# Optimization experiments

Hardware: AMD Instinct MI355X
Metric: run time of the kernel (lower is better)

## Reference

```python
import jax, jax.numpy as jnp
import numpy as np

ALPHA = 32.0
LN_EPS = 1e-5

def _cdist(a, b):
    # a: [C, M, K], b: [C, N, K] -> [C, M, N] euclidean distances
    d2 = (jnp.sum(a * a, -1)[:, :, None]
          + jnp.sum(b * b, -1)[:, None, :]
          - 2.0 * jnp.einsum('cmk,cnk->cmn', a, b))
    return jnp.sqrt(jnp.maximum(d2, 1e-12))

def setup_inputs() -> dict:
    key = jax.random.key(0)
    k1, k2 = jax.random.split(key)
    B, D, H, W, C = 8, 16, 28, 28, 256
    CN, SS = 128, 28 * 28
    x = jax.random.normal(k1, (B, D, H, W, C), dtype=jnp.float32)
    ln_weight = jnp.ones((C,), dtype=jnp.float32)
    ln_bias = jnp.zeros((C,), dtype=jnp.float32)
    cluster_center = jax.random.uniform(k2, (C, CN, SS), dtype=jnp.float32)
    return {"x": x, "ln_weight": ln_weight, "ln_bias": ln_bias,
            "cluster_center": cluster_center}

def reference(x, ln_weight, ln_bias, cluster_center):
    B, D, H, W, C = x.shape
    CN = cluster_center.shape[1]
    # LayerNorm over last dim (feature_dim)
    mu = jnp.mean(x, -1, keepdims=True)
    var = jnp.mean(jnp.square(x - mu), -1, keepdims=True)
    xn = (x - mu) * jax.lax.rsqrt(var + LN_EPS) * ln_weight + ln_bias
    # B D H W C -> C (B D) (H W)
    x_re = jnp.transpose(xn, (4, 0, 1, 2, 3)).reshape(C, B * D, H * W)
    soft_assign = _cdist(x_re, cluster_center)          # [C, B*D, CN]
    # C (B D) CN -> B D C CN
    x_distance = jnp.transpose(soft_assign.reshape(C, B, D, CN), (1, 2, 0, 3))
    # NegSoftAssign: exp(-alpha*(x - min)) normalized == softmax(-alpha*x)
    x_distance_assign = jax.nn.softmax(-ALPHA * x_distance, axis=-1)
    cluster_dist = _cdist(cluster_center, cluster_center)  # [C, CN, CN]
    return (x_distance, x_distance_assign, cluster_dist)
```

## Files before the change

kernel.cpp:

```cpp
#include <hip/hip_runtime.h>
#include <hip/hip_bf16.h>
#include <math.h>

#define C_DIM 256
#define BD    128
#define HW    784
#define CN    128
#define KPAD  832
#define KTILES 26
#define CC_BLOCKS 2048

typedef short bf16x8 __attribute__((ext_vector_type(8)));
typedef float f32x4 __attribute__((ext_vector_type(4)));

__device__ inline ushort f2b(float f) {
  unsigned u = __float_as_uint(f);
  unsigned r = (u + 0x7FFFu + ((u >> 16) & 1u)) >> 16;
  return (ushort)r;
}

__global__ __launch_bounds__(256, 5) void prep_kernel(
    const float* __restrict__ x, const float* __restrict__ lnw,
    const float* __restrict__ lnb, const float* __restrict__ cc,
    ushort* __restrict__ xre, ushort* __restrict__ ccb) {
  __shared__ __align__(16) ushort btile[256 * 32];
  const int t = threadIdx.x, bid = blockIdx.x;
  const int w = t >> 6, lane = t & 63;
  const int q = lane >> 4, l = lane & 15;

  if (bid < CC_BLOCKS) {
    const int c = bid >> 3;
    const int r = (bid & 7) * 16 + w * 4 + q;
    const float4* src = (const float4*)(cc + ((size_t)c * CN + r) * HW);
    ushort* dst = ccb + ((size_t)c * CN + r) * KPAD;
    float4 v[13];
#pragma unroll
    for (int i = 0; i < 13; ++i) {
      if (i < 12 || l < 4) v[i] = src[i * 16 + l];
    }
#pragma unroll
    for (int i = 0; i < 13; ++i) {
      if (i < 12 || l < 4) {
        ushort4 o;
        o.x = f2b(v[i].x); o.y = f2b(v[i].y);
        o.z = f2b(v[i].z); o.w = f2b(v[i].w);
        *(ushort4*)(dst + (i * 16 + l) * 4) = o;
      }
    }
    if (l < 12) *(ushort4*)(dst + 784 + l * 4) = make_ushort4(0, 0, 0, 0);
    return;
  }

  const int idx = bid - CC_BLOCKS;
  const int bx = idx % 26;
  const int bd = idx / 26;
  const int hw0 = bx * 32;

  if (bx == 25) {
#pragma unroll
    for (int i = 0; i < 8; ++i) {
      int c = w * 64 + i * 8 + (lane >> 3);
      int ho = (lane & 7) * 4;
      *(uint2*)(xre + (size_t)c * (BD * KPAD) + (size_t)bd * KPAD + hw0 + ho) =
          make_uint2(0u, 0u);
    }
    return;
  }

  const bool half = (bx == 24);
  const int ngroups = half ? 1 : 2;
  const int rpw = ngroups * 4;
  const int msk = (l & 7) << 2;

  if (half) {
    int rp2 = (16 + w * 4 + q) ^ msk;
#pragma unroll
    for (int s = 0; s < 4; ++s)
#pragma unroll
      for (int j = 0; j < 4; ++j)
        btile[(s * 64 + l * 4 + j) * 32 + rp2] = 0;
  }

  float4 wv[4], bv[4];
#pragma unroll
  for (int s = 0; s < 4; ++s) {
    wv[s] = *(const float4*)(lnw + s * 64 + l * 4);
    bv[s] = *(const float4*)(lnb + s * 64 + l * 4);
  }
  const float* xb = x + ((size_t)bd * HW + hw0) * 256 + l * 4;

#define LOADG(V, g)                                                            \
  do {                                                                         \
    int r_ = w * rpw + (g) * 4 + q;                                            \
    _Pragma("unroll") for (int s = 0; s < 4; ++s)                              \
        V[s] = *(const float4*)(xb + (size_t)r_ * 256 + s * 64);               \
  } while (0)

#define PROC(V, g)                                                             \
  do {                                                                         \
    int r_ = w * rpw + (g) * 4 + q;                                            \
    float sum = 0.f, sq = 0.f;                                                 \
    _Pragma("unroll") for (int s = 0; s < 4; ++s) {                            \
      sum += V[s].x + V[s].y + V[s].z + V[s].w;                                \
      sq = fmaf(V[s].x, V[s].x, sq); sq = fmaf(V[s].y, V[s].y, sq);            \
      sq = fmaf(V[s].z, V[s].z, sq); sq = fmaf(V[s].w, V[s].w, sq);            \
    }                                                                          \
    for (int off = 1; off <= 8; off <<= 1) {                                   \
      sum += __shfl_xor(sum, off, 64);                                         \
      sq  += __shfl_xor(sq, off, 64);                                          \
    }                                                                          \
    float mu = sum * (1.f / 256.f);                                            \
    float var = fmaf(-mu, mu, sq * (1.f / 256.f));                             \
    float sc = rsqrtf(var + 1e-5f);                                            \
    int rp_ = r_ ^ msk;                                                        \
    _Pragma("unroll") for (int s = 0; s < 4; ++s) {                            \
      float y0 = (V[s].x - mu) * sc * wv[s].x + bv[s].x;                       \
      float y1 = (V[s].y - mu) * sc * wv[s].y + bv[s].y;                       \
      float y2 = (V[s].z - mu) * sc * wv[s].z + bv[s].z;                       \
      float y3 = (V[s].w - mu) * sc * wv[s].w + bv[s].w;                       \
      int c_ = s * 64 + l * 4;                                                 \
      btile[(c_ + 0) * 32 + rp_] = f2b(y0);                                    \
      btile[(c_ + 1) * 32 + rp_] = f2b(y1);                                    \
      btile[(c_ + 2) * 32 + rp_] = f2b(y2);                                    \
      btile[(c_ + 3) * 32 + rp_] = f2b(y3);                                    \
    }                                                                          \
  } while (0)

  float4 va[4], vb[4];
  LOADG(va, 0);
  if (ngroups > 1) {
    LOADG(vb, 1);
    PROC(va, 0);
    PROC(vb, 1);
  } else {
    PROC(va, 0);
  }
#undef LOADG
#undef PROC
  __syncthreads();
#pragma unroll
  for (int i = 0; i < 8; ++i) {
    int c = w * 64 + i * 8 + (lane >> 3);
    int xw = ((c >> 2) & 7) << 2;
    int ho = (lane & 7) * 4;
    uint2 val = *(const uint2*)&btile[c * 32 + (ho ^ xw)];
    *(uint2*)(xre + (size_t)c * (BD * KPAD) + (size_t)bd * KPAD + hw0 + ho) = val;
  }
}

__global__ __launch_bounds__(256, 2) void gemm_fused_kernel(
    const ushort* __restrict__ xre, const ushort* __restrict__ ccb,
    float* __restrict__ out_d, float* __restrict__ out_s,
    float* __restrict__ out_c) {
  __shared__ __align__(16) ushort At[2][2048];
  __shared__ __align__(16) ushort Bt[2][4096];
  __shared__ float an_l[64], bn_l[128];
  const int bid = blockIdx.x;
  const int xcd = bid & 7, i6 = bid >> 3;
  const int c = xcd * 32 + (i6 >> 1);
  const int h = i6 & 1;
  const int t = threadIdx.x, w = t >> 6, lane = t & 63;
  const int quad = lane >> 4, ln = lane & 15;
  const ushort* Ag = xre + (size_t)c * (128 * KPAD) + (size_t)(h * 64) * KPAD;
  const ushort* Bg = ccb + (size_t)c * (128 * KPAD);

  f32x4 accx[8], accc[8];
  f32x4 accd  = f32x4{0.f, 0.f, 0.f, 0.f};
  f32x4 accbd = f32x4{0.f, 0.f, 0.f, 0.f};
#pragma unroll
  for (int j = 0; j < 8; ++j) {
    accx[j] = f32x4{0.f, 0.f, 0.f, 0.f};
    accc[j] = f32x4{0.f, 0.f, 0.f, 0.f};
  }

  const int srow = t >> 2, scq = (t & 3) ^ (srow & 3);
  const ushort* gA  = Ag + (size_t)srow * KPAD + scq * 8;
  const ushort* gB1 = Bg + (size_t)srow * KPAD + scq * 8;
  const ushort* gB2 = Bg + (size_t)(srow + 64) * KPAD + scq * 8;

  const int m = w * 16 + ln;
  const int aoff  = (m * 4 + (quad ^ (m & 3))) * 8;
  const int aroff = ((h * 64 + m) * 4 + (quad ^ (m & 3))) * 8;
  const int nD = (1 - h) * 64 + w * 16 + ln;
  const int bdoff = (nD * 4 + (quad ^ (nD & 3))) * 8;
  int boff[8];
#pragma unroll
  for (int j = 0; j < 8; ++j) {
    int n = j * 16 + ln;
    boff[j] = (n * 4 + (quad ^ (n & 3))) * 8;
  }

#define ISSUE(k, p)                                                            \
  do {                                                                         \
    int kb = (k) * 32;                                                         \
    __builtin_amdgcn_global_load_lds(                                          \
        (const __attribute__((address_space(1))) unsigned int*)(gA + kb),      \
        (__attribute__((address_space(3))) unsigned int*)&At[p][t * 8], 16, 0, 0); \
    __builtin_amdgcn_global_load_lds(                                          \
        (const __attribute__((address_space(1))) unsigned int*)(gB1 + kb),     \
        (__attribute__((address_space(3))) unsigned int*)&Bt[p][t * 8], 16, 0, 0); \
    __builtin_amdgcn_global_load_lds(                                          \
        (const __attribute__((address_space(1))) unsigned int*)(gB2 + kb),     \
        (__attribute__((address_space(3))) unsigned int*)&Bt[p][t * 8 + 2048], 16, 0, 0); \
  } while (0)

  ISSUE(0, 0);
  for (int k0 = 0; k0 < KTILES; ++k0) {
    __syncthreads();
    if (k0 < KTILES - 1) ISSUE(k0 + 1, (k0 + 1) & 1);
    const int p = k0 & 1;
    bf16x8 af  = *(const bf16x8*)&At[p][aoff];
    bf16x8 ar  = *(const bf16x8*)&Bt[p][aroff];
    bf16x8 bdr = *(const bf16x8*)&Bt[p][bdoff];
    accd  = __builtin_amdgcn_mfma_f32_16x16x32_bf16(af, af, accd, 0, 0, 0);
    accbd = __builtin_amdgcn_mfma_f32_16x16x32_bf16(bdr, bdr, accbd, 0, 0, 0);
#pragma unroll
    for (int j = 0; j < 8; ++j) {
      bf16x8 bfj = *(const bf16x8*)&Bt[p][boff[j]];
      accx[j] = __builtin_amdgcn_mfma_f32_16x16x32_bf16(af, bfj, accx[j], 0, 0, 0);
      accc[j] = __builtin_amdgcn_mfma_f32_16x16x32_bf16(ar, bfj, accc[j], 0, 0, 0);
    }
  }
#undef ISSUE

  if ((ln >> 2) == quad) {
#pragma unroll
    for (int r2 = 0; r2 < 4; ++r2)
      if (r2 == (ln & 3)) {
        an_l[w * 16 + ln] = accd[r2];
        bn_l[(1 - h) * 64 + w * 16 + ln] = accbd[r2];
      }
#pragma unroll
    for (int j = 0; j < 8; ++j)
      if (j == h * 4 + w) {
#pragma unroll
        for (int r2 = 0; r2 < 4; ++r2)
          if (r2 == (ln & 3))
            bn_l[h * 64 + w * 16 + ln] = accc[j][r2];
      }
  }
  __syncthreads();

  float cn[8];
#pragma unroll
  for (int j = 0; j < 8; ++j) cn[j] = bn_l[j * 16 + ln];
  float rx[4], rc[4];
#pragma unroll
  for (int r = 0; r < 4; ++r) {
    rx[r] = an_l[w * 16 + quad * 4 + r];
    rc[r] = bn_l[h * 64 + w * 16 + quad * 4 + r];
  }
#pragma unroll
  for (int r = 0; r < 4; ++r) {
    int mr = h * 64 + w * 16 + quad * 4 + r;
    float* ob = out_c + (size_t)c * (128 * 128) + (size_t)mr * 128;
#pragma unroll
    for (int j = 0; j < 8; ++j) {
      float d2 = rc[r] + cn[j] - 2.f * accc[j][r];
      ob[j * 16 + ln] = sqrtf(fmaxf(d2, 1e-12f));
    }
  }
#pragma unroll
  for (int r = 0; r < 4; ++r) {
    int mr = h * 64 + w * 16 + quad * 4 + r;
    float dr[8];
#pragma unroll
    for (int j = 0; j < 8; ++j) {
      float d2 = rx[r] + cn[j] - 2.f * accx[j][r];
      dr[j] = sqrtf(fmaxf(d2, 1e-12f));
    }
    float* ob = out_d + ((size_t)mr * 256 + c) * 128;
#pragma unroll
    for (int j = 0; j < 8; ++j) ob[j * 16 + ln] = dr[j];
    float mn = dr[0];
#pragma unroll
    for (int j = 1; j < 8; ++j) mn = fminf(mn, dr[j]);
    for (int off = 1; off <= 8; off <<= 1) mn = fminf(mn, __shfl_xor(mn, off, 64));
    float e[8], s = 0.f;
#pragma unroll
    for (int j = 0; j < 8; ++j) { e[j] = __expf(-32.f * (dr[j] - mn)); s += e[j]; }
    for (int off = 1; off <= 8; off <<= 1) s += __shfl_xor(s, off, 64);
    float inv = 1.f / s;
    float* os = out_s + ((size_t)mr * 256 + c) * 128;
#pragma unroll
    for (int j = 0; j < 8; ++j) os[j * 16 + ln] = e[j] * inv;
  }
}

extern "C" void kernel_launch(void* const* d_in, const int* in_sizes, int n_in,
                              void* d_out, int out_size, void* d_ws, size_t ws_size,
                              hipStream_t stream) {
  const float* x   = (const float*)d_in[0];
  const float* lnw = (const float*)d_in[1];
  const float* lnb = (const float*)d_in[2];
  const float* cc  = (const float*)d_in[3];
  float* out   = (float*)d_out;
  float* out_d = out;
  float* out_s = out + 4194304;
  float* out_c = out + 8388608;

  ushort* xre_b = (ushort*)d_ws;
  ushort* cc_b  = xre_b + 27262976;

  prep_kernel<<<5376, 256, 0, stream>>>(x, lnw, lnb, cc, xre_b, cc_b);
  gemm_fused_kernel<<<512, 256, 0, stream>>>(xre_b, cc_b, out_d, out_s, out_c);
}
```

Before: 306.0 us.

## Triple-buffer GEMM loads with explicit waitcnt and widen prep tiles to 64 columns

Result: faster. 297.3 us (-2.8%).

```diff
diff --git a/kernel.cpp b/kernel.cpp
--- a/kernel.cpp
+++ b/kernel.cpp
@@ -8,7 +8,6 @@
 #define CN    128
 #define KPAD  832
 #define KTILES 26
-#define CC_BLOCKS 2048
 
 typedef short bf16x8 __attribute__((ext_vector_type(8)));
 typedef float f32x4 __attribute__((ext_vector_type(4)));
@@ -19,16 +18,16 @@
   return (ushort)r;
 }
 
-__global__ __launch_bounds__(256, 5) void prep_kernel(
+__global__ __launch_bounds__(256, 4) void prep_kernel(
     const float* __restrict__ x, const float* __restrict__ lnw,
     const float* __restrict__ lnb, const float* __restrict__ cc,
     ushort* __restrict__ xre, ushort* __restrict__ ccb) {
-  __shared__ __align__(16) ushort btile[256 * 32];
+  __shared__ __align__(16) ushort btile[256 * 64];
   const int t = threadIdx.x, bid = blockIdx.x;
   const int w = t >> 6, lane = t & 63;
   const int q = lane >> 4, l = lane & 15;
 
-  if (bid < CC_BLOCKS) {
+  if (bid < 2048) {
     const int c = bid >> 3;
     const int r = (bid & 7) * 16 + w * 4 + q;
     const float4* src = (const float4*)(cc + ((size_t)c * CN + r) * HW);
@@ -51,36 +50,19 @@
     return;
   }
 
-  const int idx = bid - CC_BLOCKS;
-  const int bx = idx % 26;
-  const int bd = idx / 26;
-  const int hw0 = bx * 32;
-
-  if (bx == 25) {
-#pragma unroll
-    for (int i = 0; i < 8; ++i) {
-      int c = w * 64 + i * 8 + (lane >> 3);
-      int ho = (lane & 7) * 4;
-      *(uint2*)(xre + (size_t)c * (BD * KPAD) + (size_t)bd * KPAD + hw0 + ho) =
-          make_uint2(0u, 0u);
-    }
-    return;
-  }
-
-  const bool half = (bx == 24);
-  const int ngroups = half ? 1 : 2;
+  const int idx = bid - 2048;
+  const int bx = idx % 13;
+  const int bd = idx / 13;
+  const int hw0 = bx * 64;
+  const bool last = (bx == 12);
+  const int ngroups = last ? 1 : 4;
   const int rpw = ngroups * 4;
-  const int msk = (l & 7) << 2;
-
-  if (half) {
-    int rp2 = (16 + w * 4 + q) ^ msk;
-#pragma unroll
-    for (int s = 0; s < 4; ++s)
-#pragma unroll
-      for (int j = 0; j < 4; ++j)
-        btile[(s * 64 + l * 4 + j) * 32 + rp2] = 0;
-  }
-
+  const int xr2 = (l & 12) | ((l & 3) << 4);
+  if (last) {
+    int xf = ((t >> 2) & 12) ^ ((t & 12) << 2);
+    for (int r = 16; r < 64; r += 4)
+      *(ushort4*)&btile[t * 64 + (r ^ xf)] = make_ushort4(0, 0, 0, 0);
+  }
   float4 wv[4], bv[4];
 #pragma unroll
   for (int s = 0; s < 4; ++s) {
@@ -112,17 +94,17 @@
     float mu = sum * (1.f / 256.f);                                            \
     float var = fmaf(-mu, mu, sq * (1.f / 256.f));                             \
     float sc = rsqrtf(var + 1e-5f);                                            \
-    int rp_ = r_ ^ msk;                                                        \
+    int rp_ = r_ ^ xr2;                                                        \
     _Pragma("unroll") for (int s = 0; s < 4; ++s) {                            \
       float y0 = (V[s].x - mu) * sc * wv[s].x + bv[s].x;                       \
       float y1 = (V[s].y - mu) * sc * wv[s].y + bv[s].y;                       \
       float y2 = (V[s].z - mu) * sc * wv[s].z + bv[s].z;                       \
       float y3 = (V[s].w - mu) * sc * wv[s].w + bv[s].w;                       \
       int c_ = s * 64 + l * 4;                                                 \
-      btile[(c_ + 0) * 32 + rp_] = f2b(y0);                                    \
-      btile[(c_ + 1) * 32 + rp_] = f2b(y1);                                    \
-      btile[(c_ + 2) * 32 + rp_] = f2b(y2);                                    \
-      btile[(c_ + 3) * 32 + rp_] = f2b(y3);                                    \
+      btile[(c_ + 0) * 64 + rp_] = f2b(y0);                                    \
+      btile[(c_ + 1) * 64 + rp_] = f2b(y1);                                    \
+      btile[(c_ + 2) * 64 + rp_] = f2b(y2);                                    \
+      btile[(c_ + 3) * 64 + rp_] = f2b(y3);                                    \
     }                                                                          \
   } while (0)
 
@@ -131,7 +113,11 @@
   if (ngroups > 1) {
     LOADG(vb, 1);
     PROC(va, 0);
+    LOADG(va, 2);
     PROC(vb, 1);
+    LOADG(vb, 3);
+    PROC(va, 2);
+    PROC(vb, 3);
   } else {
     PROC(va, 0);
   }
@@ -139,11 +125,11 @@
 #undef PROC
   __syncthreads();
 #pragma unroll
-  for (int i = 0; i < 8; ++i) {
-    int c = w * 64 + i * 8 + (lane >> 3);
-    int xw = ((c >> 2) & 7) << 2;
-    int ho = (lane & 7) * 4;
-    uint2 val = *(const uint2*)&btile[c * 32 + (ho ^ xw)];
+  for (int i = 0; i < 16; ++i) {
+    int c = w * 64 + i * 4 + (lane >> 4);
+    int xw = ((c >> 2) & 12) ^ ((c & 12) << 2);
+    int ho = (lane & 15) * 4;
+    uint2 val = *(const uint2*)&btile[c * 64 + (ho ^ xw)];
     *(uint2*)(xre + (size_t)c * (BD * KPAD) + (size_t)bd * KPAD + hw0 + ho) = val;
   }
 }
@@ -152,8 +138,8 @@
     const ushort* __restrict__ xre, const ushort* __restrict__ ccb,
     float* __restrict__ out_d, float* __restrict__ out_s,
     float* __restrict__ out_c) {
-  __shared__ __align__(16) ushort At[2][2048];
-  __shared__ __align__(16) ushort Bt[2][4096];
+  __shared__ __align__(16) ushort At[3][2048];
+  __shared__ __align__(16) ushort Bt[3][4096];
   __shared__ float an_l[64], bn_l[128];
   const int bid = blockIdx.x;
   const int xcd = bid & 7, i6 = bid >> 3;
@@ -205,13 +191,23 @@
   } while (0)
 
   ISSUE(0, 0);
+  ISSUE(1, 1);
   for (int k0 = 0; k0 < KTILES; ++k0) {
-    __syncthreads();
-    if (k0 < KTILES - 1) ISSUE(k0 + 1, (k0 + 1) & 1);
-    const int p = k0 & 1;
+    const int p = k0 % 3;
+    if (k0 < KTILES - 2) {
+      ISSUE(k0 + 2, (k0 + 2) % 3);
+      asm volatile("s_waitcnt vmcnt(6)" ::: "memory");
+    } else if (k0 == KTILES - 2) {
+      asm volatile("s_waitcnt vmcnt(3)" ::: "memory");
+    } else {
+      asm volatile("s_waitcnt vmcnt(0)" ::: "memory");
+    }
+    __builtin_amdgcn_s_barrier();
+    __builtin_amdgcn_sched_barrier(0);
     bf16x8 af  = *(const bf16x8*)&At[p][aoff];
     bf16x8 ar  = *(const bf16x8*)&Bt[p][aroff];
     bf16x8 bdr = *(const bf16x8*)&Bt[p][bdoff];
+    __builtin_amdgcn_s_setprio(1);
     accd  = __builtin_amdgcn_mfma_f32_16x16x32_bf16(af, af, accd, 0, 0, 0);
     accbd = __builtin_amdgcn_mfma_f32_16x16x32_bf16(bdr, bdr, accbd, 0, 0, 0);
 #pragma unroll
@@ -220,9 +216,13 @@
       accx[j] = __builtin_amdgcn_mfma_f32_16x16x32_bf16(af, bfj, accx[j], 0, 0, 0);
       accc[j] = __builtin_amdgcn_mfma_f32_16x16x32_bf16(ar, bfj, accc[j], 0, 0, 0);
     }
+    __builtin_amdgcn_s_setprio(0);
+    asm volatile("s_waitcnt lgkmcnt(0)" ::: "memory");
+    __builtin_amdgcn_s_barrier();
   }
 #undef ISSUE
 
+  __syncthreads();
   if ((ln >> 2) == quad) {
 #pragma unroll
     for (int r2 = 0; r2 < 4; ++r2)
@@ -302,6 +302,6 @@
   ushort* xre_b = (ushort*)d_ws;
   ushort* cc_b  = xre_b + 27262976;
 
-  prep_kernel<<<5376, 256, 0, stream>>>(x, lnw, lnb, cc, xre_b, cc_b);
+  prep_kernel<<<3712, 256, 0, stream>>>(x, lnw, lnb, cc, xre_b, cc_b);
   gemm_fused_kernel<<<512, 256, 0, stream>>>(xre_b, cc_b, out_d, out_s, out_c);
 }
```

## Split LayerNorm into stats pass and wide-tile apply/transpose kernel

Applied to the files above, without the earlier changes.

New measurement: 318.3 us. +4.0%, slower.

```diff
diff --git a/kernel.cpp b/kernel.cpp
--- a/kernel.cpp
+++ b/kernel.cpp
@@ -8,7 +8,6 @@
 #define CN    128
 #define KPAD  832
 #define KTILES 26
-#define CC_BLOCKS 2048
 
 typedef short bf16x8 __attribute__((ext_vector_type(8)));
 typedef float f32x4 __attribute__((ext_vector_type(4)));
@@ -19,16 +18,14 @@
   return (ushort)r;
 }
 
-__global__ __launch_bounds__(256, 5) void prep_kernel(
-    const float* __restrict__ x, const float* __restrict__ lnw,
-    const float* __restrict__ lnb, const float* __restrict__ cc,
-    ushort* __restrict__ xre, ushort* __restrict__ ccb) {
-  __shared__ __align__(16) ushort btile[256 * 32];
+__global__ __launch_bounds__(256) void stats_cc_kernel(
+    const float* __restrict__ x, const float* __restrict__ cc,
+    float2* __restrict__ stats, ushort* __restrict__ ccb) {
   const int t = threadIdx.x, bid = blockIdx.x;
   const int w = t >> 6, lane = t & 63;
   const int q = lane >> 4, l = lane & 15;
 
-  if (bid < CC_BLOCKS) {
+  if (bid < 2048) {
     const int c = bid >> 3;
     const int r = (bid & 7) * 16 + w * 4 + q;
     const float4* src = (const float4*)(cc + ((size_t)c * CN + r) * HW);
@@ -51,54 +48,21 @@
     return;
   }
 
-  const int idx = bid - CC_BLOCKS;
-  const int bx = idx % 26;
-  const int bd = idx / 26;
-  const int hw0 = bx * 32;
-
-  if (bx == 25) {
-#pragma unroll
-    for (int i = 0; i < 8; ++i) {
-      int c = w * 64 + i * 8 + (lane >> 3);
-      int ho = (lane & 7) * 4;
-      *(uint2*)(xre + (size_t)c * (BD * KPAD) + (size_t)bd * KPAD + hw0 + ho) =
-          make_uint2(0u, 0u);
-    }
-    return;
-  }
-
-  const bool half = (bx == 24);
-  const int ngroups = half ? 1 : 2;
-  const int rpw = ngroups * 4;
-  const int msk = (l & 7) << 2;
-
-  if (half) {
-    int rp2 = (16 + w * 4 + q) ^ msk;
-#pragma unroll
-    for (int s = 0; s < 4; ++s)
-#pragma unroll
-      for (int j = 0; j < 4; ++j)
-        btile[(s * 64 + l * 4 + j) * 32 + rp2] = 0;
-  }
-
-  float4 wv[4], bv[4];
-#pragma unroll
-  for (int s = 0; s < 4; ++s) {
-    wv[s] = *(const float4*)(lnw + s * 64 + l * 4);
-    bv[s] = *(const float4*)(lnb + s * 64 + l * 4);
-  }
-  const float* xb = x + ((size_t)bd * HW + hw0) * 256 + l * 4;
-
-#define LOADG(V, g)                                                            \
+  const int sb = bid - 2048;
+  const int bd = sb / 7, tile = sb % 7;
+  const int hwbase = tile * 112;
+
+#define LOADP(V, p)                                                            \
   do {                                                                         \
-    int r_ = w * rpw + (g) * 4 + q;                                            \
-    _Pragma("unroll") for (int s = 0; s < 4; ++s)                              \
-        V[s] = *(const float4*)(xb + (size_t)r_ * 256 + s * 64);               \
+    int hw_ = hwbase + (p) * 16 + w * 4 + q;                                   \
+    const float* rp = x + ((size_t)bd * HW + hw_) * 256 + l * 4;               \
+    V[0] = *(const float4*)rp;       V[1] = *(const float4*)(rp + 64);         \
+    V[2] = *(const float4*)(rp + 128); V[3] = *(const float4*)(rp + 192);      \
   } while (0)
 
-#define PROC(V, g)                                                             \
+#define PROCP(V, p)                                                            \
   do {                                                                         \
-    int r_ = w * rpw + (g) * 4 + q;                                            \
+    int hw_ = hwbase + (p) * 16 + w * 4 + q;                                   \
     float sum = 0.f, sq = 0.f;                                                 \
     _Pragma("unroll") for (int s = 0; s < 4; ++s) {                            \
       sum += V[s].x + V[s].y + V[s].z + V[s].w;                                \
@@ -111,40 +75,86 @@
     }                                                                          \
     float mu = sum * (1.f / 256.f);                                            \
     float var = fmaf(-mu, mu, sq * (1.f / 256.f));                             \
-    float sc = rsqrtf(var + 1e-5f);                                            \
-    int rp_ = r_ ^ msk;                                                        \
-    _Pragma("unroll") for (int s = 0; s < 4; ++s) {                            \
-      float y0 = (V[s].x - mu) * sc * wv[s].x + bv[s].x;                       \
-      float y1 = (V[s].y - mu) * sc * wv[s].y + bv[s].y;                       \
-      float y2 = (V[s].z - mu) * sc * wv[s].z + bv[s].z;                       \
-      float y3 = (V[s].w - mu) * sc * wv[s].w + bv[s].w;                       \
-      int c_ = s * 64 + l * 4;                                                 \
-      btile[(c_ + 0) * 32 + rp_] = f2b(y0);                                    \
-      btile[(c_ + 1) * 32 + rp_] = f2b(y1);                                    \
-      btile[(c_ + 2) * 32 + rp_] = f2b(y2);                                    \
-      btile[(c_ + 3) * 32 + rp_] = f2b(y3);                                    \
-    }                                                                          \
+    if (l == 0)                                                                \
+      stats[(size_t)bd * HW + hw_] = make_float2(mu, rsqrtf(var + 1e-5f));     \
   } while (0)
 
   float4 va[4], vb[4];
-  LOADG(va, 0);
-  if (ngroups > 1) {
-    LOADG(vb, 1);
-    PROC(va, 0);
-    PROC(vb, 1);
-  } else {
-    PROC(va, 0);
-  }
-#undef LOADG
-#undef PROC
-  __syncthreads();
-#pragma unroll
-  for (int i = 0; i < 8; ++i) {
-    int c = w * 64 + i * 8 + (lane >> 3);
-    int xw = ((c >> 2) & 7) << 2;
-    int ho = (lane & 7) * 4;
-    uint2 val = *(const uint2*)&btile[c * 32 + (ho ^ xw)];
-    *(uint2*)(xre + (size_t)c * (BD * KPAD) + (size_t)bd * KPAD + hw0 + ho) = val;
+  LOADP(va, 0);
+  LOADP(vb, 1); PROCP(va, 0);
+  LOADP(va, 2); PROCP(vb, 1);
+  LOADP(vb, 3); PROCP(va, 2);
+  LOADP(va, 4); PROCP(vb, 3);
+  LOADP(vb, 5); PROCP(va, 4);
+  LOADP(va, 6); PROCP(vb, 5);
+  PROCP(va, 6);
+#undef LOADP
+#undef PROCP
+}
+
+__global__ __launch_bounds__(256) void apply_transpose_kernel(
+    const float* __restrict__ x, const float* __restrict__ lnw,
+    const float* __restrict__ lnb, const float2* __restrict__ stats,
+    ushort* __restrict__ xre) {
+  __shared__ __align__(16) ushort btile[64 * 256];
+  __shared__ float2 st_l[256];
+  const int t = threadIdx.x;
+  const int ct = blockIdx.x & 3, bd = blockIdx.x >> 2;
+  const int c0 = ct * 64;
+  const int tg = t >> 4, tl = t & 15;
+  const int row = t >> 2, rl = t & 3;
+  const float4 wv = *(const float4*)(lnw + c0 + tl * 4);
+  const float4 bv = *(const float4*)(lnb + c0 + tl * 4);
+  const float* xb = x + (size_t)bd * HW * 256 + c0 + tl * 4;
+  const float2* sbp = stats + (size_t)bd * HW;
+  const int cc0 = tl * 4;
+  const int rsw = (row & 15) << 2;
+
+  for (int ch = 0; ch < 4; ++ch) {
+    const int h0 = ch * 256;
+    const bool tail = (ch == 3);
+    if (!tail) st_l[t] = sbp[h0 + t];
+    else if (t < 16) st_l[t] = sbp[h0 + t];
+    __syncthreads();
+    if (tail) {
+#pragma unroll
+      for (int z = 0; z < 12; ++z) {
+        int hh = 16 + rl * 12 + z;
+        btile[row * 256 + (hh ^ rsw)] = 0;
+      }
+    }
+    const int ni = tail ? 1 : 16;
+    for (int i = 0; i < ni; ++i) {
+      int hwl = tg + i * 16;
+      float4 v = *(const float4*)(xb + (size_t)(h0 + hwl) * 256);
+      float2 s = st_l[hwl];
+      float y0 = (v.x - s.x) * s.y * wv.x + bv.x;
+      float y1 = (v.y - s.x) * s.y * wv.y + bv.y;
+      float y2 = (v.z - s.x) * s.y * wv.z + bv.z;
+      float y3 = (v.w - s.x) * s.y * wv.w + bv.w;
+      btile[(cc0 + 0) * 256 + (hwl ^ (((cc0 + 0) & 15) << 2))] = f2b(y0);
+      btile[(cc0 + 1) * 256 + (hwl ^ (((cc0 + 1) & 15) << 2))] = f2b(y1);
+      btile[(cc0 + 2) * 256 + (hwl ^ (((cc0 + 2) & 15) << 2))] = f2b(y2);
+      btile[(cc0 + 3) * 256 + (hwl ^ (((cc0 + 3) & 15) << 2))] = f2b(y3);
+    }
+    __syncthreads();
+    ushort* drow =
+        xre + (size_t)(c0 + row) * (BD * KPAD) + (size_t)bd * KPAD + h0;
+    if (!tail) {
+#pragma unroll
+      for (int i2 = 0; i2 < 16; ++i2) {
+        int hwl = rl * 64 + i2 * 4;
+        *(uint2*)(drow + hwl) =
+            *(const uint2*)&btile[row * 256 + (hwl ^ rsw)];
+      }
+    } else {
+#pragma unroll
+      for (int i2 = 0; i2 < 4; ++i2) {
+        int hwl = rl * 16 + i2 * 4;
+        *(uint2*)(drow + hwl) =
+            *(const uint2*)&btile[row * 256 + (hwl ^ rsw)];
+      }
+    }
   }
 }
 
@@ -223,6 +233,7 @@
   }
 #undef ISSUE
 
+  __syncthreads();
   if ((ln >> 2) == quad) {
 #pragma unroll
     for (int r2 = 0; r2 < 4; ++r2)
@@ -301,7 +312,9 @@
 
   ushort* xre_b = (ushort*)d_ws;
   ushort* cc_b  = xre_b + 27262976;
-
-  prep_kernel<<<5376, 256, 0, stream>>>(x, lnw, lnb, cc, xre_b, cc_b);
+  float2* stats = (float2*)(cc_b + 27262976);
+
+  stats_cc_kernel<<<2944, 256, 0, stream>>>(x, cc, stats, cc_b);
+  apply_transpose_kernel<<<512, 256, 0, stream>>>(x, lnw, lnb, stats, xre_b);
   gemm_fused_kernel<<<512, 256, 0, stream>>>(xre_b, cc_b, out_d, out_s, out_c);
 }
```
